# Kernel optimization log

Hardware: AMD Instinct MI355X
Metric: run time of the kernel (lower is better)

Reference implementation:

```python
import jax, jax.numpy as jnp
import numpy as np


def setup_inputs() -> dict:
    key = jax.random.key(0)
    ks = jax.random.split(key, 10)
    B, T, E, H, HS, V = 4, 1024, 1024, 16, 64, 32000
    D = H * HS
    s = 0.02  # init scale to keep logits numerically sane
    return {
        "x": jax.random.randint(ks[0], (B, T), 0, V, dtype=jnp.int64) if jax.config.jax_enable_x64 else jax.random.randint(ks[0], (B, T), 0, V, dtype=jnp.int32),
        "y": jax.random.randint(ks[1], (B, T), 0, V, dtype=jnp.int32),
        "tok_emb": jax.random.normal(ks[2], (V, E), jnp.float32) * s,
        "pos_emb": jax.random.normal(ks[3], (T, E), jnp.float32) * s,
        "Wq": jax.random.normal(ks[4], (H, E, HS), jnp.float32) * s,
        "Wk": jax.random.normal(ks[5], (H, E, HS), jnp.float32) * s,
        "Wv": jax.random.normal(ks[6], (H, E, HS), jnp.float32) * s,
        "ff_w": jax.random.normal(ks[7], (D, D), jnp.float32) * s,
        "ff_b": jnp.zeros((D,), jnp.float32),
        "fc_w": jax.random.normal(ks[8], (D, V), jnp.float32) * s,
        "fc_b": jnp.zeros((V,), jnp.float32),
    }


def reference(x, y, tok_emb, pos_emb, Wq, Wk, Wv, ff_w, ff_b, fc_w, fc_b):
    B, T = x.shape
    HS = Wq.shape[-1]
    h = tok_emb[x] + pos_emb[:T]                       # [B,T,E]
    q = jnp.einsum('bte,hed->bhtd', h, Wq)             # [B,H,T,HS]
    k = jnp.einsum('bte,hed->bhtd', h, Wk)
    v = jnp.einsum('bte,hed->bhtd', h, Wv)
    # NOTE: original code multiplies by 1/(head_size**-0.5) == sqrt(head_size)
    scores = jnp.einsum('bhtd,bhsd->bhts', q, k) * (HS ** 0.5)
    mask = jnp.tril(jnp.ones((T, T), dtype=bool))      # causal
    scores = jnp.where(mask, scores, -jnp.inf)
    attn = jax.nn.softmax(scores, axis=-1)
    o = jnp.einsum('bhts,bhsd->bhtd', attn, v)         # [B,H,T,HS]
    o = o.transpose(0, 2, 1, 3).reshape(B, T, -1)      # concat heads -> [B,T,D]
    ff = jax.nn.relu(o @ ff_w + ff_b)                  # [B,T,D]
    logits = ff @ fc_w + fc_b                          # [B,T,V]
    V = logits.shape[-1]
    logits = logits.reshape(B * T, V)
    logp = jax.nn.log_softmax(logits, axis=-1)
    loss = -jnp.take_along_axis(logp, y.reshape(B * T, 1), axis=-1).mean()
    return logits, loss
```

## Files before the change

kernel.cpp:

```cpp
#include <hip/hip_runtime.h>


typedef __bf16 bf16x8 __attribute__((ext_vector_type(8)));
typedef float f32x4 __attribute__((ext_vector_type(4)));
typedef unsigned short u16;

#define MFMA16(a, b, c) __builtin_amdgcn_mfma_f32_16x16x32_bf16(a, b, c, 0, 0, 0)

__device__ __forceinline__ u16 f2bf(float f) {
    union { float f; unsigned int u; } v; v.f = f;
    unsigned int r = v.u + 0x7fffu + ((v.u >> 16) & 1u);
    return (u16)(r >> 16);
}

__device__ __forceinline__ void gld16(const u16* g, u16* l) {
    __builtin_amdgcn_global_load_lds((__attribute__((address_space(1))) void*)g,
                                     (__attribute__((address_space(3))) void*)l,
                                     16, 0, 0);
}

__global__ void embed_kernel(const int* __restrict__ x, const float* __restrict__ tok,
                             const float* __restrict__ pos, u16* __restrict__ h) {
    int bt = blockIdx.x;
    int t = bt & 1023;
    int row = x[bt];
    const float* te = tok + (size_t)row * 1024;
    const float* pe = pos + (size_t)t * 1024;
    int c = threadIdx.x * 4;
    float4 a = *(const float4*)(te + c);
    float4 b = *(const float4*)(pe + c);
    union { u16 s[4]; uint2 v; } o;
    o.s[0] = f2bf(a.x + b.x); o.s[1] = f2bf(a.y + b.y);
    o.s[2] = f2bf(a.z + b.z); o.s[3] = f2bf(a.w + b.w);
    *(uint2*)(h + (size_t)bt * 1024 + c) = o.v;
}

__global__ void transpose_f32_bf16(const float* __restrict__ src, u16* __restrict__ dst,
                                   int R, int C) {
    __shared__ float tile[64][65];
    const float* s = src + (size_t)blockIdx.z * R * C;
    u16* d = dst + (size_t)blockIdx.z * R * C;
    int r0 = blockIdx.x * 64, c0 = blockIdx.y * 64;
    int tr = threadIdx.x >> 2, tg = threadIdx.x & 3;
#pragma unroll
    for (int i = 0; i < 4; i++) {
        float4 v = *(const float4*)(s + (size_t)(r0 + tr) * C + c0 + tg * 16 + i * 4);
        tile[tr][tg * 16 + i * 4 + 0] = v.x;
        tile[tr][tg * 16 + i * 4 + 1] = v.y;
        tile[tr][tg * 16 + i * 4 + 2] = v.z;
        tile[tr][tg * 16 + i * 4 + 3] = v.w;
    }
    __syncthreads();
    union { u16 s[16]; uint4 v[2]; } pk;
#pragma unroll
    for (int i = 0; i < 16; i++) pk.s[i] = f2bf(tile[tg * 16 + i][tr]);
    u16* dp = d + (size_t)(c0 + tr) * R + r0 + tg * 16;
    *(uint4*)(dp) = pk.v[0];
    *(uint4*)(dp + 8) = pk.v[1];
}

template <int MODE>
__global__ __launch_bounds__(256, 2) void gemm_bt(const u16* __restrict__ A,
                                                  const u16* __restrict__ Bt,
                                                  void* __restrict__ Cout,
                                                  const float* __restrict__ bias,
                                                  int M, int N, int K) {
    __shared__ __align__(16) u16 As[128 * 64];
    __shared__ __align__(16) u16 Bs[128 * 64];
    int tid = threadIdx.x, lane = tid & 63, wave = tid >> 6;
    int quad = lane >> 4, ln = lane & 15;
    int m0 = blockIdx.x * 128, n0 = blockIdx.y * 128;
    int wm = (wave & 1) * 64, wn = (wave >> 1) * 64;
    f32x4 acc[4][4] = {};

    for (int k0 = 0; k0 < K; k0 += 64) {
        __syncthreads();
#pragma unroll
        for (int c = 0; c < 4; c++) {
            int chunk = c * 256 + wave * 64 + lane;
            int r = chunk >> 3, kc = chunk & 7;
            gld16(A + (size_t)(m0 + r) * K + k0 + kc * 8, As + chunk * 8);
            gld16(Bt + (size_t)(n0 + r) * K + k0 + kc * 8, Bs + chunk * 8);
        }
        __syncthreads();
        bf16x8 af[4][2], bf[4][2];
#pragma unroll
        for (int i = 0; i < 4; i++) {
#pragma unroll
            for (int kk = 0; kk < 2; kk++) {
                af[i][kk] = *(const bf16x8*)(As + (wm + i * 16 + ln) * 64 + kk * 32 + quad * 8);
                bf[i][kk] = *(const bf16x8*)(Bs + (wn + i * 16 + ln) * 64 + kk * 32 + quad * 8);
            }
        }
#pragma unroll
        for (int i = 0; i < 4; i++)
#pragma unroll
            for (int j = 0; j < 4; j++) {
                acc[i][j] = MFMA16(af[i][0], bf[j][0], acc[i][j]);
                acc[i][j] = MFMA16(af[i][1], bf[j][1], acc[i][j]);
            }
    }

#pragma unroll
    for (int i = 0; i < 4; i++)
#pragma unroll
        for (int j = 0; j < 4; j++) {
            int col = n0 + wn + j * 16 + ln;
            float bv = (MODE >= 1) ? bias[col] : 0.f;
#pragma unroll
            for (int r = 0; r < 4; r++) {
                int row = m0 + wm + i * 16 + quad * 4 + r;
                float v = acc[i][j][r] + bv;
                if (MODE == 1) v = fmaxf(v, 0.f);
                if (MODE == 2) {
                    ((float*)Cout)[(size_t)row * N + col] = v;
                } else {
                    ((u16*)Cout)[(size_t)row * N + col] = f2bf(v);
                }
            }
        }
}

__global__ __launch_bounds__(256, 2) void attn_kernel(const u16* __restrict__ qkv,
                                                      u16* __restrict__ o) {
    __shared__ __align__(16) u16 kt[64 * 64];
    __shared__ __align__(16) u16 vt[64 * 64];
    __shared__ __align__(16) u16 pt[4][16 * 64];
    int tid = threadIdx.x, lane = tid & 63, wave = tid >> 6;
    int quad = lane >> 4, ln = lane & 15;
    int it = blockIdx.x;
    int b = blockIdx.y >> 4, hh = blockIdx.y & 15;
    int t0 = it * 64;

    bf16x8 qf[2];
    {
        const u16* qb = qkv + (size_t)(b * 1024 + t0 + wave * 16 + ln) * 3072 + hh * 64 + quad * 8;
        qf[0] = *(const bf16x8*)(qb);
        qf[1] = *(const bf16x8*)(qb + 32);
    }
    f32x4 Oacc[4] = {};
    float m_run[4], l_run[4];
#pragma unroll
    for (int r = 0; r < 4; r++) { m_run[r] = -1e30f; l_run[r] = 0.f; }

    for (int j = 0; j <= it; j++) {
        __syncthreads();
        {
            int r = tid >> 2, cg = tid & 3;
            const u16* krow = qkv + (size_t)(b * 1024 + j * 64 + r) * 3072 + 1024 + hh * 64 + cg * 16;
            uint4 k0 = *(const uint4*)(krow);
            uint4 k1 = *(const uint4*)(krow + 8);
            *(uint4*)(kt + r * 64 + cg * 16) = k0;
            *(uint4*)(kt + r * 64 + cg * 16 + 8) = k1;
            union { uint4 v; u16 s[8]; } v0, v1;
            v0.v = *(const uint4*)(krow + 1024);
            v1.v = *(const uint4*)(krow + 1024 + 8);
#pragma unroll
            for (int i = 0; i < 8; i++) vt[(cg * 16 + i) * 64 + r] = v0.s[i];
#pragma unroll
            for (int i = 0; i < 8; i++) vt[(cg * 16 + 8 + i) * 64 + r] = v1.s[i];
        }
        __syncthreads();

        f32x4 S[4];
#pragma unroll
        for (int ct = 0; ct < 4; ct++) {
            f32x4 s = {};
            bf16x8 kf0 = *(const bf16x8*)(kt + (ct * 16 + ln) * 64 + quad * 8);
            bf16x8 kf1 = *(const bf16x8*)(kt + (ct * 16 + ln) * 64 + 32 + quad * 8);
            s = MFMA16(qf[0], kf0, s);
            s = MFMA16(qf[1], kf1, s);
            S[ct] = s;
        }
#pragma unroll
        for (int ct = 0; ct < 4; ct++)
#pragma unroll
            for (int r = 0; r < 4; r++) {
                int srow = t0 + wave * 16 + quad * 4 + r;
                int scol = j * 64 + ct * 16 + ln;
                S[ct][r] = (scol <= srow) ? S[ct][r] * 8.0f : -1e30f;
            }
        float alpha[4];
#pragma unroll
        for (int r = 0; r < 4; r++) {
            float mx = fmaxf(fmaxf(S[0][r], S[1][r]), fmaxf(S[2][r], S[3][r]));
#pragma unroll
            for (int off = 1; off < 16; off <<= 1) mx = fmaxf(mx, __shfl_xor(mx, off, 16));
            float mn = fmaxf(m_run[r], mx);
            alpha[r] = __expf(m_run[r] - mn);
            float ssum = 0.f;
#pragma unroll
            for (int ct = 0; ct < 4; ct++) {
                float p = __expf(S[ct][r] - mn);
                S[ct][r] = p;
                ssum += p;
            }
#pragma unroll
            for (int off = 1; off < 16; off <<= 1) ssum += __shfl_xor(ssum, off, 16);
            l_run[r] = l_run[r] * alpha[r] + ssum;
            m_run[r] = mn;
        }
        u16* ptw = pt[wave];
#pragma unroll
        for (int ct = 0; ct < 4; ct++)
#pragma unroll
            for (int r = 0; r < 4; r++)
                ptw[(quad * 4 + r) * 64 + ct * 16 + ln] = f2bf(S[ct][r]);
#pragma unroll
        for (int dt = 0; dt < 4; dt++)
#pragma unroll
            for (int r = 0; r < 4; r++) Oacc[dt][r] *= alpha[r];
        bf16x8 pf0 = *(const bf16x8*)(ptw + ln * 64 + quad * 8);
        bf16x8 pf1 = *(const bf16x8*)(ptw + ln * 64 + 32 + quad * 8);
#pragma unroll
        for (int dt = 0; dt < 4; dt++) {
            bf16x8 vf0 = *(const bf16x8*)(vt + (dt * 16 + ln) * 64 + quad * 8);
            bf16x8 vf1 = *(const bf16x8*)(vt + (dt * 16 + ln) * 64 + 32 + quad * 8);
            Oacc[dt] = MFMA16(pf0, vf0, Oacc[dt]);
            Oacc[dt] = MFMA16(pf1, vf1, Oacc[dt]);
        }
    }
#pragma unroll
    for (int r = 0; r < 4; r++) l_run[r] = 1.0f / l_run[r];
#pragma unroll
    for (int dt = 0; dt < 4; dt++)
#pragma unroll
        for (int r = 0; r < 4; r++) {
            int row = b * 1024 + t0 + wave * 16 + quad * 4 + r;
            o[(size_t)row * 1024 + hh * 64 + dt * 16 + ln] = f2bf(Oacc[dt][r] * l_run[r]);
        }
}

__global__ __launch_bounds__(256) void loss_row(const float* __restrict__ logits,
                                                const int* __restrict__ y,
                                                float* __restrict__ rl) {
    int row = blockIdx.x;
    const float* z = logits + (size_t)row * 32000;
    float m = -1e30f, s = 0.f;
    for (int i = threadIdx.x; i < 32000; i += 256) {
        float v = z[i];
        float mn = fmaxf(m, v);
        s = s * __expf(m - mn) + __expf(v - mn);
        m = mn;
    }
#pragma unroll
    for (int off = 1; off < 64; off <<= 1) {
        float m2 = __shfl_xor(m, off);
        float s2 = __shfl_xor(s, off);
        float mn = fmaxf(m, m2);
        s = s * __expf(m - mn) + s2 * __expf(m2 - mn);
        m = mn;
    }
    __shared__ float sm[4], ss[4];
    int wave = threadIdx.x >> 6;
    if ((threadIdx.x & 63) == 0) { sm[wave] = m; ss[wave] = s; }
    __syncthreads();
    if (threadIdx.x == 0) {
        float M = sm[0], S = ss[0];
#pragma unroll
        for (int w = 1; w < 4; w++) {
            float mn = fmaxf(M, sm[w]);
            S = S * __expf(M - mn) + ss[w] * __expf(sm[w] - mn);
            M = mn;
        }
        rl[row] = (M + __logf(S)) - z[y[row]];
    }
}

__global__ void loss_final(const float* __restrict__ rl, float* __restrict__ out) {
    float s = 0.f;
    for (int i = threadIdx.x; i < 4096; i += 256) s += rl[i];
#pragma unroll
    for (int off = 1; off < 64; off <<= 1) s += __shfl_xor(s, off);
    __shared__ float a[4];
    if ((threadIdx.x & 63) == 0) a[threadIdx.x >> 6] = s;
    __syncthreads();
    if (threadIdx.x == 0) out[0] = (a[0] + a[1] + a[2] + a[3]) * (1.0f / 4096.0f);
}

extern "C" void kernel_launch(void* const* d_in, const int* in_sizes, int n_in,
                              void* d_out, int out_size, void* d_ws, size_t ws_size,
                              hipStream_t stream) {
    const int* x = (const int*)d_in[0];
    const int* y = (const int*)d_in[1];
    const float* tok = (const float*)d_in[2];
    const float* pos = (const float*)d_in[3];
    const float* Wq = (const float*)d_in[4];
    const float* Wk = (const float*)d_in[5];
    const float* Wv = (const float*)d_in[6];
    const float* ffw = (const float*)d_in[7];
    const float* ffb = (const float*)d_in[8];
    const float* fcw = (const float*)d_in[9];
    const float* fcb = (const float*)d_in[10];
    float* out = (float*)d_out;

    u16* ws = (u16*)d_ws;
    u16* h = ws;
    u16* wqkvt = h + (size_t)4096 * 1024;
    u16* qkv = wqkvt + (size_t)3072 * 1024;
    u16* oo = qkv + (size_t)4096 * 3072;
    u16* ffwt = oo + (size_t)4096 * 1024;
    u16* ffact = ffwt + (size_t)1024 * 1024;
    u16* fcwt = ffact + (size_t)4096 * 1024;
    float* rowloss = (float*)(fcwt + (size_t)32000 * 1024);

    embed_kernel<<<4096, 256, 0, stream>>>(x, tok, pos, h);

    transpose_f32_bf16<<<dim3(16, 1, 16), 256, 0, stream>>>(Wq, wqkvt, 1024, 64);
    transpose_f32_bf16<<<dim3(16, 1, 16), 256, 0, stream>>>(Wk, wqkvt + (size_t)1024 * 1024, 1024, 64);
    transpose_f32_bf16<<<dim3(16, 1, 16), 256, 0, stream>>>(Wv, wqkvt + (size_t)2048 * 1024, 1024, 64);
    transpose_f32_bf16<<<dim3(16, 16, 1), 256, 0, stream>>>(ffw, ffwt, 1024, 1024);
    transpose_f32_bf16<<<dim3(16, 500, 1), 256, 0, stream>>>(fcw, fcwt, 1024, 32000);

    gemm_bt<0><<<dim3(32, 24), 256, 0, stream>>>(h, wqkvt, qkv, nullptr, 4096, 3072, 1024);

    attn_kernel<<<dim3(16, 64), 256, 0, stream>>>(qkv, oo);

    gemm_bt<1><<<dim3(32, 8), 256, 0, stream>>>(oo, ffwt, ffact, ffb, 4096, 1024, 1024);

    gemm_bt<2><<<dim3(32, 250), 256, 0, stream>>>(ffact, fcwt, out, fcb, 4096, 32000, 1024);

    loss_row<<<4096, 256, 0, stream>>>(out, y, rowloss);
    loss_final<<<1, 256, 0, stream>>>(rowloss, out + (size_t)4096 * 32000);
}
```

Before: 1.313 ms.

## Replace vocab GEMM with 256x256 pipelined kernel fusing partial log-sum-exp

Result: faster. 1.124 ms (-14.4%).

```diff
diff --git a/kernel.cpp b/kernel.cpp
--- a/kernel.cpp
+++ b/kernel.cpp
@@ -6,6 +6,14 @@
 typedef unsigned short u16;
 
 #define MFMA16(a, b, c) __builtin_amdgcn_mfma_f32_16x16x32_bf16(a, b, c, 0, 0, 0)
+#define SCHED_FENCE() __builtin_amdgcn_sched_barrier(0)
+#define SBAR()                        \
+    do {                              \
+        SCHED_FENCE();                \
+        __builtin_amdgcn_s_barrier(); \
+        SCHED_FENCE();                \
+    } while (0)
+#define VMW(N) asm volatile("s_waitcnt vmcnt(" #N ")" ::: "memory")
 
 __device__ __forceinline__ u16 f2bf(float f) {
     union { float f; unsigned int u; } v; v.f = f;
@@ -112,13 +120,167 @@
                 int row = m0 + wm + i * 16 + quad * 4 + r;
                 float v = acc[i][j][r] + bv;
                 if (MODE == 1) v = fmaxf(v, 0.f);
-                if (MODE == 2) {
-                    ((float*)Cout)[(size_t)row * N + col] = v;
-                } else {
-                    ((u16*)Cout)[(size_t)row * N + col] = f2bf(v);
-                }
+                ((u16*)Cout)[(size_t)row * N + col] = f2bf(v);
             }
         }
+}
+
+__device__ __forceinline__ void ldA4(bf16x8 (&fa)[4][2], const u16* p0, const u16* p1, int off) {
+#pragma unroll
+    for (int ii = 0; ii < 4; ++ii) {
+        fa[ii][0] = *(const bf16x8*)(p0 + off + ii * 1024);
+        fa[ii][1] = *(const bf16x8*)(p1 + off + ii * 1024);
+    }
+}
+__device__ __forceinline__ void ldB2(bf16x8 (&fb)[2][2], const u16* p0, const u16* p1, int off) {
+#pragma unroll
+    for (int jj = 0; jj < 2; ++jj) {
+        fb[jj][0] = *(const bf16x8*)(p0 + off + jj * 1024);
+        fb[jj][1] = *(const bf16x8*)(p1 + off + jj * 1024);
+    }
+}
+__device__ __forceinline__ void mfma_quad(f32x4 (&acc)[8][4], const bf16x8 (&A)[4][2],
+                                          const bf16x8 (&B)[2][2], int qr, int qc) {
+    __builtin_amdgcn_s_setprio(1);
+#pragma unroll
+    for (int ii = 0; ii < 4; ++ii)
+#pragma unroll
+        for (int jj = 0; jj < 2; ++jj) {
+            f32x4 c = acc[qr * 4 + ii][qc * 2 + jj];
+            c = MFMA16(A[ii][0], B[jj][0], c);
+            c = MFMA16(A[ii][1], B[jj][1], c);
+            acc[qr * 4 + ii][qc * 2 + jj] = c;
+        }
+    __builtin_amdgcn_s_setprio(0);
+}
+
+__global__ __launch_bounds__(512, 2) void gemm256_lse(const u16* __restrict__ A,
+                                                      const u16* __restrict__ Bt,
+                                                      float* __restrict__ C,
+                                                      const float* __restrict__ bias,
+                                                      float2* __restrict__ pl,
+                                                      int M, int N, int K) {
+    __shared__ __align__(16) u16 lds[65536];
+    const int tid = threadIdx.x;
+    const int lane = tid & 63;
+    const int wave = tid >> 6;
+    const int quad = lane >> 4, ln = lane & 15;
+    const int wm = wave >> 2, wn = wave & 3;
+
+    const int bid = blockIdx.x;
+    const int mtile = bid & 15, ntile = bid >> 4;
+    const int m0 = mtile << 8, n0 = ntile << 8;
+
+    auto stageA = [&](int h, int b, int kt) {
+#pragma unroll
+        for (int l = 0; l < 2; ++l) {
+            int chunk = l * 512 + tid;
+            int r = chunk >> 3, kc = chunk & 7;
+            int kcs = kc ^ (r & 7);
+            gld16(A + (size_t)(m0 + h * 128 + r) * K + kt * 64 + kcs * 8,
+                  lds + h * 16384 + b * 8192 + chunk * 8);
+        }
+    };
+    auto stageB = [&](int h, int b, int kt) {
+#pragma unroll
+        for (int l = 0; l < 2; ++l) {
+            int chunk = l * 512 + tid;
+            int r = chunk >> 3, kc = chunk & 7;
+            int kcs = kc ^ (r & 7);
+            gld16(Bt + (size_t)(n0 + h * 128 + r) * K + kt * 64 + kcs * 8,
+                  lds + 32768 + h * 16384 + b * 8192 + chunk * 8);
+        }
+    };
+
+    const int c80 = ((0 * 4 + quad) ^ (ln & 7)) * 8;
+    const int c81 = ((1 * 4 + quad) ^ (ln & 7)) * 8;
+    const u16* pA0 = lds + wm * 16384 + ln * 64 + c80;
+    const u16* pA1 = lds + wm * 16384 + ln * 64 + c81;
+    const u16* pB0 = lds + 32768 + (wn >> 1) * 16384 + ((wn & 1) * 64 + ln) * 64 + c80;
+    const u16* pB1 = lds + 32768 + (wn >> 1) * 16384 + ((wn & 1) * 64 + ln) * 64 + c81;
+
+    f32x4 acc[8][4] = {};
+
+    stageA(0, 0, 0); stageA(1, 0, 0); stageB(0, 0, 0); stageB(1, 0, 0);
+    stageB(0, 1, 1); stageB(1, 1, 1); stageA(0, 1, 1);
+    VMW(6);
+    SBAR();
+
+    const int NIT = K >> 7;
+#pragma unroll 1
+    for (int j = 0; j < NIT; ++j) {
+        const int t0 = 2 * j;
+        const bool pf = (j < NIT - 1);
+        bf16x8 fa[4][2], fbA[2][2], fbB[2][2];
+
+        ldA4(fa, pA0, pA1, 0);
+        ldB2(fbA, pB0, pB1, 0);
+        stageA(1, 1, t0 + 1);
+        SBAR();
+        mfma_quad(acc, fa, fbA, 0, 0);
+        SBAR();
+        ldB2(fbB, pB0, pB1, 2048);
+        SBAR();
+        mfma_quad(acc, fa, fbB, 0, 1);
+        SBAR();
+        ldA4(fa, pA0, pA1, 4096);
+        if (pf) stageB(0, 0, t0 + 2);
+        SBAR();
+        mfma_quad(acc, fa, fbB, 1, 1);
+        SBAR();
+        if (pf) { stageB(1, 0, t0 + 2); stageA(0, 0, t0 + 2); }
+        SBAR();
+        mfma_quad(acc, fa, fbA, 1, 0);
+        if (pf) { VMW(6); } else { VMW(0); }
+        SBAR();
+
+        ldA4(fa, pA0, pA1, 8192);
+        ldB2(fbA, pB0, pB1, 8192);
+        if (pf) stageA(1, 0, t0 + 2);
+        SBAR();
+        mfma_quad(acc, fa, fbA, 0, 0);
+        SBAR();
+        ldB2(fbB, pB0, pB1, 8192 + 2048);
+        SBAR();
+        mfma_quad(acc, fa, fbB, 0, 1);
+        SBAR();
+        ldA4(fa, pA0, pA1, 8192 + 4096);
+        if (pf) stageB(0, 1, t0 + 3);
+        SBAR();
+        mfma_quad(acc, fa, fbB, 1, 1);
+        SBAR();
+        if (pf) { stageB(1, 1, t0 + 3); stageA(0, 1, t0 + 3); }
+        SBAR();
+        mfma_quad(acc, fa, fbA, 1, 0);
+        if (pf) VMW(6);
+        SBAR();
+    }
+
+    const int strips = N >> 6;
+    float bv[4];
+#pragma unroll
+    for (int jj = 0; jj < 4; ++jj) bv[jj] = bias[n0 + wn * 64 + jj * 16 + ln];
+
+#pragma unroll
+    for (int ii = 0; ii < 8; ++ii) {
+#pragma unroll
+        for (int rr = 0; rr < 4; ++rr) {
+            int row = m0 + wm * 128 + ii * 16 + quad * 4 + rr;
+            float v0 = acc[ii][0][rr] + bv[0];
+            float v1 = acc[ii][1][rr] + bv[1];
+            float v2 = acc[ii][2][rr] + bv[2];
+            float v3 = acc[ii][3][rr] + bv[3];
+            float* cp = C + (size_t)row * N + n0 + wn * 64 + ln;
+            cp[0] = v0; cp[16] = v1; cp[32] = v2; cp[48] = v3;
+            float mx = fmaxf(fmaxf(v0, v1), fmaxf(v2, v3));
+#pragma unroll
+            for (int off = 1; off < 16; off <<= 1) mx = fmaxf(mx, __shfl_xor(mx, off, 16));
+            float s = __expf(v0 - mx) + __expf(v1 - mx) + __expf(v2 - mx) + __expf(v3 - mx);
+#pragma unroll
+            for (int off = 1; off < 16; off <<= 1) s += __shfl_xor(s, off, 16);
+            if (ln == 0) pl[(size_t)row * strips + (ntile << 2) + wn] = make_float2(mx, s);
+        }
+    }
 }
 
 __global__ __launch_bounds__(256, 2) void attn_kernel(const u16* __restrict__ qkv,
@@ -231,16 +393,17 @@
         }
 }
 
-__global__ __launch_bounds__(256) void loss_row(const float* __restrict__ logits,
+__global__ __launch_bounds__(256) void lse_loss(const float2* __restrict__ pl,
+                                                const float* __restrict__ logits,
                                                 const int* __restrict__ y,
                                                 float* __restrict__ rl) {
     int row = blockIdx.x;
-    const float* z = logits + (size_t)row * 32000;
+    const float2* p = pl + (size_t)row * 500;
     float m = -1e30f, s = 0.f;
-    for (int i = threadIdx.x; i < 32000; i += 256) {
-        float v = z[i];
-        float mn = fmaxf(m, v);
-        s = s * __expf(m - mn) + __expf(v - mn);
+    for (int i = threadIdx.x; i < 500; i += 256) {
+        float2 v = p[i];
+        float mn = fmaxf(m, v.x);
+        s = s * __expf(m - mn) + v.y * __expf(v.x - mn);
         m = mn;
     }
 #pragma unroll
@@ -252,8 +415,8 @@
         m = mn;
     }
     __shared__ float sm[4], ss[4];
-    int wave = threadIdx.x >> 6;
-    if ((threadIdx.x & 63) == 0) { sm[wave] = m; ss[wave] = s; }
+    int wv = threadIdx.x >> 6;
+    if ((threadIdx.x & 63) == 0) { sm[wv] = m; ss[wv] = s; }
     __syncthreads();
     if (threadIdx.x == 0) {
         float M = sm[0], S = ss[0];
@@ -263,7 +426,7 @@
             S = S * __expf(M - mn) + ss[w] * __expf(sm[w] - mn);
             M = mn;
         }
-        rl[row] = (M + __logf(S)) - z[y[row]];
+        rl[row] = (M + __logf(S)) - logits[(size_t)row * 32000 + y[row]];
     }
 }
 
@@ -302,7 +465,8 @@
     u16* ffwt = oo + (size_t)4096 * 1024;
     u16* ffact = ffwt + (size_t)1024 * 1024;
     u16* fcwt = ffact + (size_t)4096 * 1024;
-    float* rowloss = (float*)(fcwt + (size_t)32000 * 1024);
+    float2* pl = (float2*)(fcwt + (size_t)32000 * 1024);
+    float* rowloss = (float*)(pl + (size_t)4096 * 500);
 
     embed_kernel<<<4096, 256, 0, stream>>>(x, tok, pos, h);
 
@@ -318,8 +482,8 @@
 
     gemm_bt<1><<<dim3(32, 8), 256, 0, stream>>>(oo, ffwt, ffact, ffb, 4096, 1024, 1024);
 
-    gemm_bt<2><<<dim3(32, 250), 256, 0, stream>>>(ffact, fcwt, out, fcb, 4096, 32000, 1024);
-
-    loss_row<<<4096, 256, 0, stream>>>(out, y, rowloss);
+    gemm256_lse<<<2000, 512, 0, stream>>>(ffact, fcwt, out, fcb, pl, 4096, 32000, 1024);
+
+    lse_loss<<<4096, 256, 0, stream>>>(pl, out, y, rowloss);
     loss_final<<<1, 256, 0, stream>>>(rowloss, out + (size_t)4096 * 32000);
 }
```
